# Kernel tuning notes

Measured on AMD Instinct MI355X. Metric: run time of the kernel, lower is better.

## Reference

```python
import jax, jax.numpy as jnp
import numpy as np

D_MODEL = 512
D_STATE = 16
EXPAND = 2
DT_RANK = 8
D_INNER = EXPAND * D_MODEL  # 1024
LN_EPS = 1e-5


def setup_inputs() -> dict:
    key = jax.random.key(0)
    ks = jax.random.split(key, 10)
    B, H, W = 8, 48, 48
    inp = {
        "x": jax.random.normal(ks[0], (B, H, W, D_MODEL), jnp.float32),
        # Linear weights stored [in, out] (torch weight transposed)
        "W_in": jax.random.normal(ks[1], (D_MODEL, 2 * D_INNER), jnp.float32) * 0.02,
        # depthwise conv kernel, HWIO with feature_group_count = D_INNER
        "conv_k": jax.random.normal(ks[2], (3, 3, 1, D_INNER), jnp.float32) * 0.1,
        "W_xproj": jax.random.normal(ks[3], (D_INNER, DT_RANK + 2 * D_STATE), jnp.float32) * 0.02,
        "W_dt": jax.random.uniform(ks[4], (DT_RANK, D_INNER), jnp.float32, -0.1, 0.1),
        "b_dt": jnp.full((D_INNER,), 0.1, jnp.float32),
        "A_log": jax.random.normal(ks[5], (D_STATE,), jnp.float32) * 0.02,
        "Dskip": jnp.ones((D_INNER,), jnp.float32),
        "W_dtN": jax.random.normal(ks[6], (D_INNER, D_STATE), jnp.float32) * 0.02,
        "b_dtN": jnp.zeros((D_STATE,), jnp.float32),
        "ln_g": jnp.ones((D_INNER,), jnp.float32),
        "ln_b": jnp.zeros((D_INNER,), jnp.float32),
        "W_out": jax.random.normal(ks[7], (D_INNER, D_MODEL), jnp.float32) * 0.02,
        "b_out": jnp.zeros((D_MODEL,), jnp.float32),
    }
    return inp


def _ss2d(x, W_in, conv_k, W_xproj, W_dt, b_dt, A_log, Dskip, W_dtN, b_dtN,
          ln_g, ln_b, W_out, b_out):
    B, H, W_, _ = x.shape
    L = H * W_
    # in_proj and split into x / gate z
    xz = x @ W_in                                   # [B,H,W,2*D_INNER]
    xh, z = jnp.split(xz, 2, axis=-1)
    # depthwise 3x3 conv (NHWC)
    xc = jax.lax.conv_general_dilated(
        xh, conv_k, window_strides=(1, 1), padding='SAME',
        dimension_numbers=('NHWC', 'HWIO', 'NHWC'),
        feature_group_count=D_INNER)                 # [B,H,W,D_INNER]
    # x_proj -> (dt_rank, B, C)
    xp = xc @ W_xproj
    dt_r = xp[..., :DT_RANK]
    Bp = xp[..., DT_RANK:DT_RANK + D_STATE]
    Cp = xp[..., DT_RANK + D_STATE:]
    dt = dt_r @ W_dt + b_dt                          # [B,H,W,D_INNER]
    # flatten spatial dims into sequence
    x_seq = xc.reshape(B, L, D_INNER)
    dt_seq = jax.nn.softplus(dt.reshape(B, L, D_INNER))
    B_seq = Bp.reshape(B, L, D_STATE)
    C_seq = Cp.reshape(B, L, D_STATE)
    A = -jnp.exp(A_log)                              # [N]; A_log expanded over D is constant per-row
    dtN = dt_seq @ W_dtN + b_dtN                     # dt_to_N_proj(softplus(dt)) -> [B,L,N]

    def step(h, t):
        x_t, dt_t, dtN_t, B_t, C_t = t               # [B,D],[B,D],[B,N],[B,N],[B,N]
        dA = jnp.exp(dt_t[:, :, None] * A)           # [B,D,N]
        dB = dtN_t * B_t                             # [B,N]
        h = dA * h + dB[:, None, :] * x_t[:, :, None]  # [B,D,N]
        y = jnp.einsum('bdn,bn->bd', h, C_t) + Dskip * x_t
        return h, y

    h0 = jnp.zeros((B, D_INNER, D_STATE), x.dtype)
    xs = (x_seq.transpose(1, 0, 2), dt_seq.transpose(1, 0, 2),
          dtN.transpose(1, 0, 2), B_seq.transpose(1, 0, 2),
          C_seq.transpose(1, 0, 2))
    _, ys = jax.lax.scan(step, h0, xs)               # ys: [L,B,D]
    y = ys.transpose(1, 0, 2).reshape(B, H, W_, D_INNER)
    # LayerNorm over channel dim
    mu = y.mean(-1, keepdims=True)
    var = ((y - mu) ** 2).mean(-1, keepdims=True)
    y = (y - mu) / jnp.sqrt(var + LN_EPS) * ln_g + ln_b
    # gate and out projection (dropout = identity in eval)
    y = y * jax.nn.silu(z)
    return y @ W_out + b_out


def reference(x, W_in, conv_k, W_xproj, W_dt, b_dt, A_log, Dskip, W_dtN,
              b_dtN, ln_g, ln_b, W_out, b_out):
    return _ss2d(x, W_in, conv_k, W_xproj, W_dt, b_dt, A_log, Dskip, W_dtN,
                 b_dtN, ln_g, ln_b, W_out, b_out)
```

## Files before the change

kernel.cpp:

```cpp
#include <hip/hip_runtime.h>
#include <hip/hip_bf16.h>

#define NBATCH 8
#define HEIGHT 48
#define WIDTH  48
#define DMODEL 512
#define DSTATE 16
#define DTRANK 8
#define DINNER 1024
#define LSEQ   (HEIGHT*WIDTH)
#define NROWS  (NBATCH*LSEQ)
#define NXP    40
#define NCH    32
#define TCH    72

typedef unsigned short u16;
typedef unsigned int   u32;
typedef __attribute__((ext_vector_type(8))) short short8;
typedef __attribute__((ext_vector_type(4))) float f32x4;

__device__ __forceinline__ float bf2f(u16 u) {
    u32 x = ((u32)u) << 16;
    return __uint_as_float(x);
}
__device__ __forceinline__ u16 f2bf(float f) {
    u32 x = __float_as_uint(f);
    u32 r = (x + 0x7FFFu + ((x >> 16) & 1u)) >> 16;
    return (u16)r;
}

#if __has_builtin(__builtin_amdgcn_exp2f)
__device__ __forceinline__ float EXP2(float x) { return __builtin_amdgcn_exp2f(x); }
#else
__device__ __forceinline__ float EXP2(float x) { return __expf(x * 0.69314718f); }
#endif

#define GLD16(g, l) __builtin_amdgcn_global_load_lds( \
    (const __attribute__((address_space(1))) void*)(g), \
    (__attribute__((address_space(3))) void*)(l), 16, 0, 0)

__global__ __launch_bounds__(256) void k_prep_x(const float* __restrict__ x,
                                                u16* __restrict__ xbf) {
    int i = blockIdx.x * 256 + threadIdx.x;
    float4 v = *reinterpret_cast<const float4*>(x + (size_t)i * 4);
    ushort4 o;
    o.x = f2bf(v.x); o.y = f2bf(v.y); o.z = f2bf(v.z); o.w = f2bf(v.w);
    *reinterpret_cast<ushort4*>(xbf + (size_t)i * 4) = o;
}

__global__ __launch_bounds__(256) void k_prep_w(const float* __restrict__ W_in,
                                                const float* __restrict__ W_out,
                                                const float* __restrict__ W_xproj,
                                                const float* __restrict__ W_dtN,
                                                u16* __restrict__ WinT,
                                                u16* __restrict__ WoutT,
                                                u16* __restrict__ WxpB,
                                                u16* __restrict__ WdtNB) {
    int idx = blockIdx.x * 256 + threadIdx.x;
    if (idx < 2048 * 512) {
        int n = idx >> 9, k = idx & 511;
        WinT[idx] = f2bf(W_in[(size_t)k * 2048 + n]);
    } else if (idx < 2048 * 512 + 512 * 1024) {
        int j = idx - 2048 * 512;
        int n = j >> 10, k = j & 1023;
        WoutT[j] = f2bf(W_out[(size_t)k * 512 + n]);
    } else if (idx < 2048 * 512 + 512 * 1024 + 48 * 1024) {
        int j = idx - (2048 * 512 + 512 * 1024);
        int n = j >> 10, k = j & 1023;
        WxpB[j] = (n < NXP) ? f2bf(W_xproj[(size_t)k * NXP + n]) : (u16)0;
    } else {
        int j = idx - (2048 * 512 + 512 * 1024 + 48 * 1024);
        int n = j >> 10, k = j & 1023;
        WdtNB[j] = f2bf(W_dtN[(size_t)k * DSTATE + n]);
    }
}

template<int K, int LDA, int LDB, int LDC, bool F32OUT>
__global__ __launch_bounds__(256) void k_gemm_mfma(const u16* __restrict__ A,
                                                   const u16* __restrict__ B,
                                                   const float* __restrict__ bias,
                                                   void* __restrict__ Cv) {
    __shared__ u16 As[128 * 32];
    __shared__ u16 Bs[128 * 32];
    const int tid = threadIdx.x;
    const int l   = tid & 63;
    const int w   = tid >> 6;
    const int wm  = w >> 1, wn = w & 1;
    const int m0  = blockIdx.y * 128, n0 = blockIdx.x * 128;
    const int srow = w * 32 + (l >> 2);
    const int sc   = l & 3;
    const int kh = l >> 4;
    const int lr = l & 15;

    f32x4 acc[4][4];
#pragma unroll
    for (int i = 0; i < 4; ++i)
#pragma unroll
        for (int j = 0; j < 4; ++j)
            acc[i][j] = (f32x4){0.f, 0.f, 0.f, 0.f};

    for (int k0 = 0; k0 < K; k0 += 32) {
#pragma unroll
        for (int i = 0; i < 2; ++i) {
            int r  = srow + i * 16;
            int cg = sc ^ ((r >> 1) & 3);
            const u16* ga = A + (size_t)(m0 + r) * LDA + k0 + cg * 8;
            const u16* gb = B + (size_t)(n0 + r) * LDB + k0 + cg * 8;
            GLD16(ga, As + (w * 2 + i) * 512);
            GLD16(gb, Bs + (w * 2 + i) * 512);
        }
        __syncthreads();
        short8 af[4], bfr[4];
#pragma unroll
        for (int f = 0; f < 4; ++f) {
            int ar = wm * 64 + f * 16 + lr;
            af[f]  = *reinterpret_cast<const short8*>(As + ar * 32 + ((kh ^ ((ar >> 1) & 3)) * 8));
            int br = wn * 64 + f * 16 + lr;
            bfr[f] = *reinterpret_cast<const short8*>(Bs + br * 32 + ((kh ^ ((br >> 1) & 3)) * 8));
        }
#pragma unroll
        for (int fm = 0; fm < 4; ++fm)
#pragma unroll
            for (int fn = 0; fn < 4; ++fn)
                acc[fm][fn] = __builtin_amdgcn_mfma_f32_16x16x32_bf16(
                    af[fm], bfr[fn], acc[fm][fn], 0, 0, 0);
        __syncthreads();
    }

#pragma unroll
    for (int fm = 0; fm < 4; ++fm) {
#pragma unroll
        for (int r = 0; r < 4; ++r) {
            int row = m0 + wm * 64 + fm * 16 + (l >> 4) * 4 + r;
#pragma unroll
            for (int fn = 0; fn < 4; ++fn) {
                int col = n0 + wn * 64 + fn * 16 + lr;
                if (F32OUT) {
                    ((float*)Cv)[(size_t)row * LDC + col] = acc[fm][fn][r] + bias[col];
                } else {
                    ((u16*)Cv)[(size_t)row * LDC + col] = f2bf(acc[fm][fn][r]);
                }
            }
        }
    }
}

__global__ __launch_bounds__(256) void k_conv(const u16* __restrict__ xz,
                                              const float* __restrict__ ck,
                                              u16* __restrict__ xc) {
    int row = blockIdx.x;
    int w = row % WIDTH;
    int hb = row / WIDTH;
    int h = hb % HEIGHT;
    int b = hb / HEIGHT;
    int c0 = threadIdx.x * 4;
    float a0 = 0.f, a1 = 0.f, a2 = 0.f, a3 = 0.f;
#pragma unroll
    for (int kh = 0; kh < 3; ++kh) {
        int hh = h + kh - 1;
        if (hh < 0 || hh >= HEIGHT) continue;
#pragma unroll
        for (int kw = 0; kw < 3; ++kw) {
            int ww = w + kw - 1;
            if (ww < 0 || ww >= WIDTH) continue;
            int r = (b * HEIGHT + hh) * WIDTH + ww;
            ushort4 v = *reinterpret_cast<const ushort4*>(xz + (size_t)r * 2048 + c0);
            float4 kv = *reinterpret_cast<const float4*>(ck + (kh * 3 + kw) * DINNER + c0);
            a0 = fmaf(bf2f(v.x), kv.x, a0);
            a1 = fmaf(bf2f(v.y), kv.y, a1);
            a2 = fmaf(bf2f(v.z), kv.z, a2);
            a3 = fmaf(bf2f(v.w), kv.w, a3);
        }
    }
    ushort4 ov;
    ov.x = f2bf(a0); ov.y = f2bf(a1); ov.z = f2bf(a2); ov.w = f2bf(a3);
    *reinterpret_cast<ushort4*>(xc + (size_t)row * DINNER + c0) = ov;
}

__global__ __launch_bounds__(256) void k_xproj(const u16* __restrict__ xc,
                                               const u16* __restrict__ WxpB,
                                               float* __restrict__ xp_out) {
    __shared__ u16 As[64 * 32];
    __shared__ u16 Bs[48 * 32];
    const int tid = threadIdx.x;
    const int l = tid & 63;
    const int w = tid >> 6;
    const int m0 = blockIdx.x * 64;
    const int kh = l >> 4, lr = l & 15;
    const int srow = w * 16 + (l >> 2);
    const int sc = l & 3;

    f32x4 acc[3];
    acc[0] = acc[1] = acc[2] = (f32x4){0.f, 0.f, 0.f, 0.f};

    for (int k0 = 0; k0 < 1024; k0 += 32) {
        {
            int cg = sc ^ ((srow >> 1) & 3);
            GLD16(xc + (size_t)(m0 + srow) * DINNER + k0 + cg * 8, As + w * 512);
            if (w < 3)
                GLD16(WxpB + (size_t)srow * 1024 + k0 + cg * 8, Bs + w * 512);
        }
        __syncthreads();
        int ar = w * 16 + lr;
        short8 af = *reinterpret_cast<const short8*>(As + ar * 32 + ((kh ^ ((ar >> 1) & 3)) * 8));
#pragma unroll
        for (int fn = 0; fn < 3; ++fn) {
            int br = fn * 16 + lr;
            short8 bf = *reinterpret_cast<const short8*>(Bs + br * 32 + ((kh ^ ((br >> 1) & 3)) * 8));
            acc[fn] = __builtin_amdgcn_mfma_f32_16x16x32_bf16(af, bf, acc[fn], 0, 0, 0);
        }
        __syncthreads();
    }
#pragma unroll
    for (int fn = 0; fn < 3; ++fn)
#pragma unroll
        for (int r = 0; r < 4; ++r) {
            int row = m0 + w * 16 + (l >> 4) * 4 + r;
            int col = fn * 16 + lr;
            if (col < NXP) xp_out[(size_t)row * NXP + col] = acc[fn][r];
        }
}

__global__ __launch_bounds__(256) void k_dt(const float* __restrict__ xp,
                                            const float* __restrict__ W_dt,
                                            const float* __restrict__ b_dt,
                                            u16* __restrict__ dt_out) {
    int gid = blockIdx.x * 256 + threadIdx.x;
    int row = gid >> 7;
    int dj  = (gid & 127) * 8;
    const float* xr = xp + (size_t)row * NXP;
    float4 xa = *reinterpret_cast<const float4*>(xr);
    float4 xb = *reinterpret_cast<const float4*>(xr + 4);
    float xv[8] = {xa.x, xa.y, xa.z, xa.w, xb.x, xb.y, xb.z, xb.w};
    float a[8];
    {
        float4 b0 = *reinterpret_cast<const float4*>(b_dt + dj);
        float4 b1 = *reinterpret_cast<const float4*>(b_dt + dj + 4);
        a[0]=b0.x; a[1]=b0.y; a[2]=b0.z; a[3]=b0.w;
        a[4]=b1.x; a[5]=b1.y; a[6]=b1.z; a[7]=b1.w;
    }
#pragma unroll
    for (int j = 0; j < 8; ++j) {
        float4 w0 = *reinterpret_cast<const float4*>(W_dt + j * DINNER + dj);
        float4 w1 = *reinterpret_cast<const float4*>(W_dt + j * DINNER + dj + 4);
        a[0] = fmaf(xv[j], w0.x, a[0]); a[1] = fmaf(xv[j], w0.y, a[1]);
        a[2] = fmaf(xv[j], w0.z, a[2]); a[3] = fmaf(xv[j], w0.w, a[3]);
        a[4] = fmaf(xv[j], w1.x, a[4]); a[5] = fmaf(xv[j], w1.y, a[5]);
        a[6] = fmaf(xv[j], w1.z, a[6]); a[7] = fmaf(xv[j], w1.w, a[7]);
    }
    short8 o;
#pragma unroll
    for (int j = 0; j < 8; ++j) {
        float dt = fmaxf(a[j], 0.f) + log1pf(__expf(-fabsf(a[j])));
        o[j] = (short)f2bf(dt);
    }
    *reinterpret_cast<short8*>(dt_out + (size_t)row * DINNER + dj) = o;
}

__global__ __launch_bounds__(256) void k_dtn(const u16* __restrict__ dtb,
                                             const u16* __restrict__ WdtNB,
                                             const float* __restrict__ b_dtN,
                                             const float* __restrict__ xp,
                                             float* __restrict__ dnBC) {
    __shared__ u16 As[64 * 32];
    __shared__ u16 Bs[16 * 32];
    const int tid = threadIdx.x;
    const int l = tid & 63;
    const int w = tid >> 6;
    const int m0 = blockIdx.x * 64;
    const int kh = l >> 4, lr = l & 15;
    const int srow = w * 16 + (l >> 2);
    const int sc = l & 3;

    f32x4 acc = (f32x4){0.f, 0.f, 0.f, 0.f};

    for (int k0 = 0; k0 < 1024; k0 += 32) {
        {
            int cg = sc ^ ((srow >> 1) & 3);
            GLD16(dtb + (size_t)(m0 + srow) * DINNER + k0 + cg * 8, As + w * 512);
            if (w == 0)
                GLD16(WdtNB + (size_t)srow * 1024 + k0 + cg * 8, Bs);
        }
        __syncthreads();
        int ar = w * 16 + lr;
        short8 af = *reinterpret_cast<const short8*>(As + ar * 32 + ((kh ^ ((ar >> 1) & 3)) * 8));
        short8 bf = *reinterpret_cast<const short8*>(Bs + lr * 32 + ((kh ^ ((lr >> 1) & 3)) * 8));
        acc = __builtin_amdgcn_mfma_f32_16x16x32_bf16(af, bf, acc, 0, 0, 0);
        __syncthreads();
    }
    float bn = b_dtN[lr];
#pragma unroll
    for (int r = 0; r < 4; ++r) {
        int row = m0 + w * 16 + (l >> 4) * 4 + r;
        float dn = acc[r] + bn;
        float Bv = xp[(size_t)row * NXP + DTRANK + lr];
        float Cv = xp[(size_t)row * NXP + DTRANK + DSTATE + lr];
        dnBC[(size_t)row * 32 + lr]      = dn * Bv;
        dnBC[(size_t)row * 32 + 16 + lr] = Cv;
    }
}

__global__ __launch_bounds__(256) void k_scan_p1(const u16* __restrict__ xc,
                                                 const u16* __restrict__ dtb,
                                                 const float* __restrict__ dnBC,
                                                 const float* __restrict__ A_log,
                                                 float* __restrict__ Pbuf,
                                                 float* __restrict__ Qbuf) {
    const int tid = threadIdx.x;
    const int blk = blockIdx.x;
    const int quarter = blk & 3;
    const int bc = blk >> 2;
    const int c = bc & (NCH - 1);
    const int b = bc >> 5;
    const int d = quarter * 256 + tid;

    float An2[16];
#pragma unroll
    for (int n = 0; n < 16; ++n)
        An2[n] = -__expf(A_log[n]) * 1.44269504f;

    float h[16];
#pragma unroll
    for (int n = 0; n < 16; ++n) h[n] = 0.f;
    float sdt = 0.f;

    const size_t row0 = (size_t)b * LSEQ + (size_t)c * TCH;
#pragma unroll 4
    for (int t = 0; t < TCH; ++t) {
        size_t row = row0 + t;
        float dt = bf2f(dtb[row * DINNER + d]);
        float xt = bf2f(xc[row * DINNER + d]);
        const float4* dv = reinterpret_cast<const float4*>(dnBC + row * 32);
        float4 u0 = dv[0], u1 = dv[1], u2 = dv[2], u3 = dv[3];
        sdt += dt;
        float u[16] = {u0.x,u0.y,u0.z,u0.w, u1.x,u1.y,u1.z,u1.w,
                       u2.x,u2.y,u2.z,u2.w, u3.x,u3.y,u3.z,u3.w};
#pragma unroll
        for (int n = 0; n < 16; ++n) {
            float dA = EXP2(dt * An2[n]);
            h[n] = fmaf(dA, h[n], u[n] * xt);
        }
    }
    size_t base = ((size_t)bc << 14) + d;
#pragma unroll
    for (int n = 0; n < 16; ++n) {
        Pbuf[base + (size_t)n * DINNER] = EXP2(sdt * An2[n]);
        Qbuf[base + (size_t)n * DINNER] = h[n];
    }
}

__global__ __launch_bounds__(256) void k_scan_p2(const float* __restrict__ Pbuf,
                                                 float* __restrict__ Qbuf) {
    int tid = blockIdx.x * 256 + threadIdx.x;
    int b = tid >> 14, rem = tid & 16383;
    float h = 0.f;
    for (int c = 0; c < NCH; ++c) {
        size_t idx = ((size_t)(b * NCH + c) << 14) + rem;
        float P = Pbuf[idx];
        float q = Qbuf[idx];
        Qbuf[idx] = h;
        h = fmaf(P, h, q);
    }
}

__global__ __launch_bounds__(256) void k_scan_p3(const u16* __restrict__ xc,
                                                 const u16* __restrict__ dtb,
                                                 const float* __restrict__ dnBC,
                                                 const float* __restrict__ A_log,
                                                 const float* __restrict__ Dskip,
                                                 const float* __restrict__ Qbuf,
                                                 u16* __restrict__ ybuf) {
    const int tid = threadIdx.x;
    const int blk = blockIdx.x;
    const int quarter = blk & 3;
    const int bc = blk >> 2;
    const int c = bc & (NCH - 1);
    const int b = bc >> 5;
    const int d = quarter * 256 + tid;

    float An2[16];
#pragma unroll
    for (int n = 0; n < 16; ++n)
        An2[n] = -__expf(A_log[n]) * 1.44269504f;

    float h[16];
    size_t base = ((size_t)bc << 14) + d;
#pragma unroll
    for (int n = 0; n < 16; ++n) h[n] = Qbuf[base + (size_t)n * DINNER];
    float Dsk = Dskip[d];

    const size_t row0 = (size_t)b * LSEQ + (size_t)c * TCH;
#pragma unroll 2
    for (int t = 0; t < TCH; ++t) {
        size_t row = row0 + t;
        float dt = bf2f(dtb[row * DINNER + d]);
        float xt = bf2f(xc[row * DINNER + d]);
        const float4* sv = reinterpret_cast<const float4*>(dnBC + row * 32);
        float4 u0 = sv[0], u1 = sv[1], u2 = sv[2], u3 = sv[3];
        float4 c0 = sv[4], c1 = sv[5], c2 = sv[6], c3 = sv[7];
        float u[16]  = {u0.x,u0.y,u0.z,u0.w, u1.x,u1.y,u1.z,u1.w,
                        u2.x,u2.y,u2.z,u2.w, u3.x,u3.y,u3.z,u3.w};
        float cv[16] = {c0.x,c0.y,c0.z,c0.w, c1.x,c1.y,c1.z,c1.w,
                        c2.x,c2.y,c2.z,c2.w, c3.x,c3.y,c3.z,c3.w};
        float ys[4] = {Dsk * xt, 0.f, 0.f, 0.f};
#pragma unroll
        for (int n = 0; n < 16; ++n) {
            float dA = EXP2(dt * An2[n]);
            h[n] = fmaf(dA, h[n], u[n] * xt);
            ys[n & 3] = fmaf(h[n], cv[n], ys[n & 3]);
        }
        ybuf[row * 2048 + d] = f2bf((ys[0] + ys[1]) + (ys[2] + ys[3]));
    }
}

__global__ __launch_bounds__(256) void k_ln_gate(u16* __restrict__ xz,
                                                 const float* __restrict__ ln_g,
                                                 const float* __restrict__ ln_b) {
    __shared__ float red[8];
    int row = blockIdx.x, tid = threadIdx.x;
    u16* yrow = xz + (size_t)row * 2048;
    int c0 = tid * 4;
    ushort4 v = *reinterpret_cast<const ushort4*>(yrow + c0);
    float y0 = bf2f(v.x), y1 = bf2f(v.y), y2 = bf2f(v.z), y3 = bf2f(v.w);
    float s = y0 + y1 + y2 + y3;
    float q = y0 * y0 + y1 * y1 + y2 * y2 + y3 * y3;
#pragma unroll
    for (int m = 32; m; m >>= 1) {
        s += __shfl_xor(s, m, 64);
        q += __shfl_xor(q, m, 64);
    }
    int lane = tid & 63, wv = tid >> 6;
    if (lane == 0) { red[wv] = s; red[4 + wv] = q; }
    __syncthreads();
    s = red[0] + red[1] + red[2] + red[3];
    q = red[4] + red[5] + red[6] + red[7];
    float mu = s * (1.f / DINNER);
    float var = q * (1.f / DINNER) - mu * mu;
    float rstd = rsqrtf(var + 1e-5f);
    ushort4 zv = *reinterpret_cast<const ushort4*>(yrow + DINNER + c0);
    float4 lg = *reinterpret_cast<const float4*>(ln_g + c0);
    float4 lb = *reinterpret_cast<const float4*>(ln_b + c0);
    float z0 = bf2f(zv.x), z1 = bf2f(zv.y), z2 = bf2f(zv.z), z3 = bf2f(zv.w);
    float g0 = ((y0 - mu) * rstd * lg.x + lb.x) * (z0 / (1.f + __expf(-z0)));
    float g1 = ((y1 - mu) * rstd * lg.y + lb.y) * (z1 / (1.f + __expf(-z1)));
    float g2 = ((y2 - mu) * rstd * lg.z + lb.z) * (z2 / (1.f + __expf(-z2)));
    float g3 = ((y3 - mu) * rstd * lg.w + lb.w) * (z3 / (1.f + __expf(-z3)));
    ushort4 ov;
    ov.x = f2bf(g0); ov.y = f2bf(g1); ov.z = f2bf(g2); ov.w = f2bf(g3);
    *reinterpret_cast<ushort4*>(yrow + c0) = ov;
}

extern "C" void kernel_launch(void* const* d_in, const int* in_sizes, int n_in,
                              void* d_out, int out_size, void* d_ws, size_t ws_size,
                              hipStream_t stream) {
    const float* x       = (const float*)d_in[0];
    const float* W_in    = (const float*)d_in[1];
    const float* conv_k  = (const float*)d_in[2];
    const float* W_xproj = (const float*)d_in[3];
    const float* W_dt    = (const float*)d_in[4];
    const float* b_dt    = (const float*)d_in[5];
    const float* A_log   = (const float*)d_in[6];
    const float* Dskip   = (const float*)d_in[7];
    const float* W_dtN   = (const float*)d_in[8];
    const float* b_dtN   = (const float*)d_in[9];
    const float* ln_g    = (const float*)d_in[10];
    const float* ln_b    = (const float*)d_in[11];
    const float* W_out   = (const float*)d_in[12];
    const float* b_out   = (const float*)d_in[13];
    float* out = (float*)d_out;

    char* ws = (char*)d_ws;
    size_t off = 0;
    u16*   xz    = (u16*)(ws + off); off += (size_t)NROWS * 2048 * 2;
    u16*   xc    = (u16*)(ws + off); off += (size_t)NROWS * 1024 * 2;
    u16*   dtb   = (u16*)(ws + off); off += (size_t)NROWS * 1024 * 2;
    float* xpb   = (float*)(ws + off); off += (size_t)NROWS * NXP * 4;
    float* dnBC  = (float*)(ws + off); off += (size_t)NROWS * 32 * 4;
    char*  scr   = ws + off; off += 2 * (size_t)NBATCH * NCH * DINNER * DSTATE * 4;
    u16*   xbf   = (u16*)scr;
    float* Pbuf  = (float*)scr;
    float* Qbuf  = (float*)(scr + (size_t)NBATCH * NCH * DINNER * DSTATE * 4);
    u16*   WinT  = (u16*)(ws + off); off += (size_t)2048 * 512 * 2;
    u16*   WoutT = (u16*)(ws + off); off += (size_t)512 * 1024 * 2;
    u16*   WxpB  = (u16*)(ws + off); off += (size_t)48 * 1024 * 2;
    u16*   WdtNB = (u16*)(ws + off); off += (size_t)16 * 1024 * 2;

    k_prep_x<<<(NROWS * DMODEL / 4) / 256, 256, 0, stream>>>(x, xbf);
    k_prep_w<<<(2048 * 512 + 512 * 1024 + 48 * 1024 + 16 * 1024) / 256, 256, 0, stream>>>(
        W_in, W_out, W_xproj, W_dtN, WinT, WoutT, WxpB, WdtNB);
    k_gemm_mfma<512, 512, 512, 2048, false>
        <<<dim3(2048 / 128, NROWS / 128), 256, 0, stream>>>(xbf, WinT, nullptr, xz);
    k_conv<<<NROWS, 256, 0, stream>>>(xz, conv_k, xc);
    k_xproj<<<NROWS / 64, 256, 0, stream>>>(xc, WxpB, xpb);
    k_dt<<<(NROWS * DINNER / 8) / 256, 256, 0, stream>>>(xpb, W_dt, b_dt, dtb);
    k_dtn<<<NROWS / 64, 256, 0, stream>>>(dtb, WdtNB, b_dtN, xpb, dnBC);
    k_scan_p1<<<NBATCH * NCH * 4, 256, 0, stream>>>(xc, dtb, dnBC, A_log,
                                                    Pbuf, Qbuf);
    k_scan_p2<<<(NBATCH * DINNER * DSTATE) / 256, 256, 0, stream>>>(Pbuf, Qbuf);
    k_scan_p3<<<NBATCH * NCH * 4, 256, 0, stream>>>(xc, dtb, dnBC, A_log,
                                                    Dskip, Qbuf, xz);
    k_ln_gate<<<NROWS, 256, 0, stream>>>(xz, ln_g, ln_b);
    k_gemm_mfma<1024, 2048, 1024, 512, true>
        <<<dim3(DMODEL / 128, NROWS / 128), 256, 0, stream>>>(xz, WoutT, b_out, out);
}
```

Measured before the change: 363.1 us.

## Split scan state dimension across two half-waves to double scan parallelism

The chunked scan kernels (p1 and p3) now split the 16 state components between two 32-lane halves of each wavefront, so each thread carries 8 states instead of 16, and the grid doubles to 8 blocks per (batch, chunk). In p3 the partial outputs are combined with a cross-half shuffle and only one half writes y. This halves per-thread serial work and register pressure and doubles the number of blocks, at the cost of duplicated dt/x loads and extra shuffles.

```diff
diff --git a/kernel.cpp b/kernel.cpp
--- a/kernel.cpp
+++ b/kernel.cpp
@@ -308,20 +308,25 @@
                                                  float* __restrict__ Qbuf) {
     const int tid = threadIdx.x;
     const int blk = blockIdx.x;
-    const int quarter = blk & 3;
-    const int bc = blk >> 2;
+    const int oct = blk & 7;
+    const int bc  = blk >> 3;
     const int c = bc & (NCH - 1);
     const int b = bc >> 5;
-    const int d = quarter * 256 + tid;
-
-    float An2[16];
-#pragma unroll
-    for (int n = 0; n < 16; ++n)
-        An2[n] = -__expf(A_log[n]) * 1.44269504f;
-
-    float h[16];
-#pragma unroll
-    for (int n = 0; n < 16; ++n) h[n] = 0.f;
+    const int w = tid >> 6;
+    const int lane = tid & 63;
+    const int dL = lane & 31;
+    const int nh = lane >> 5;
+    const int d = oct * 128 + w * 32 + dL;
+    const int nb = nh * 8;
+
+    float An2[8];
+#pragma unroll
+    for (int j = 0; j < 8; ++j)
+        An2[j] = -__expf(A_log[nb + j]) * 1.44269504f;
+
+    float h[8];
+#pragma unroll
+    for (int j = 0; j < 8; ++j) h[j] = 0.f;
     float sdt = 0.f;
 
     const size_t row0 = (size_t)b * LSEQ + (size_t)c * TCH;
@@ -330,22 +335,21 @@
         size_t row = row0 + t;
         float dt = bf2f(dtb[row * DINNER + d]);
         float xt = bf2f(xc[row * DINNER + d]);
-        const float4* dv = reinterpret_cast<const float4*>(dnBC + row * 32);
-        float4 u0 = dv[0], u1 = dv[1], u2 = dv[2], u3 = dv[3];
+        const float4* dv = reinterpret_cast<const float4*>(dnBC + row * 32 + nb);
+        float4 u0 = dv[0], u1 = dv[1];
         sdt += dt;
-        float u[16] = {u0.x,u0.y,u0.z,u0.w, u1.x,u1.y,u1.z,u1.w,
-                       u2.x,u2.y,u2.z,u2.w, u3.x,u3.y,u3.z,u3.w};
-#pragma unroll
-        for (int n = 0; n < 16; ++n) {
-            float dA = EXP2(dt * An2[n]);
-            h[n] = fmaf(dA, h[n], u[n] * xt);
-        }
-    }
-    size_t base = ((size_t)bc << 14) + d;
-#pragma unroll
-    for (int n = 0; n < 16; ++n) {
-        Pbuf[base + (size_t)n * DINNER] = EXP2(sdt * An2[n]);
-        Qbuf[base + (size_t)n * DINNER] = h[n];
+        float u[8] = {u0.x, u0.y, u0.z, u0.w, u1.x, u1.y, u1.z, u1.w};
+#pragma unroll
+        for (int j = 0; j < 8; ++j) {
+            float dA = EXP2(dt * An2[j]);
+            h[j] = fmaf(dA, h[j], u[j] * xt);
+        }
+    }
+    size_t base = ((size_t)bc << 14) + (size_t)nb * DINNER + d;
+#pragma unroll
+    for (int j = 0; j < 8; ++j) {
+        Pbuf[base + (size_t)j * DINNER] = EXP2(sdt * An2[j]);
+        Qbuf[base + (size_t)j * DINNER] = h[j];
     }
 }
 
@@ -372,21 +376,26 @@
                                                  u16* __restrict__ ybuf) {
     const int tid = threadIdx.x;
     const int blk = blockIdx.x;
-    const int quarter = blk & 3;
-    const int bc = blk >> 2;
+    const int oct = blk & 7;
+    const int bc  = blk >> 3;
     const int c = bc & (NCH - 1);
     const int b = bc >> 5;
-    const int d = quarter * 256 + tid;
-
-    float An2[16];
-#pragma unroll
-    for (int n = 0; n < 16; ++n)
-        An2[n] = -__expf(A_log[n]) * 1.44269504f;
-
-    float h[16];
-    size_t base = ((size_t)bc << 14) + d;
-#pragma unroll
-    for (int n = 0; n < 16; ++n) h[n] = Qbuf[base + (size_t)n * DINNER];
+    const int w = tid >> 6;
+    const int lane = tid & 63;
+    const int dL = lane & 31;
+    const int nh = lane >> 5;
+    const int d = oct * 128 + w * 32 + dL;
+    const int nb = nh * 8;
+
+    float An2[8];
+#pragma unroll
+    for (int j = 0; j < 8; ++j)
+        An2[j] = -__expf(A_log[nb + j]) * 1.44269504f;
+
+    float h[8];
+    size_t base = ((size_t)bc << 14) + (size_t)nb * DINNER + d;
+#pragma unroll
+    for (int j = 0; j < 8; ++j) h[j] = Qbuf[base + (size_t)j * DINNER];
     float Dsk = Dskip[d];
 
     const size_t row0 = (size_t)b * LSEQ + (size_t)c * TCH;
@@ -395,21 +404,22 @@
         size_t row = row0 + t;
         float dt = bf2f(dtb[row * DINNER + d]);
         float xt = bf2f(xc[row * DINNER + d]);
-        const float4* sv = reinterpret_cast<const float4*>(dnBC + row * 32);
-        float4 u0 = sv[0], u1 = sv[1], u2 = sv[2], u3 = sv[3];
-        float4 c0 = sv[4], c1 = sv[5], c2 = sv[6], c3 = sv[7];
-        float u[16]  = {u0.x,u0.y,u0.z,u0.w, u1.x,u1.y,u1.z,u1.w,
-                        u2.x,u2.y,u2.z,u2.w, u3.x,u3.y,u3.z,u3.w};
-        float cv[16] = {c0.x,c0.y,c0.z,c0.w, c1.x,c1.y,c1.z,c1.w,
-                        c2.x,c2.y,c2.z,c2.w, c3.x,c3.y,c3.z,c3.w};
-        float ys[4] = {Dsk * xt, 0.f, 0.f, 0.f};
-#pragma unroll
-        for (int n = 0; n < 16; ++n) {
-            float dA = EXP2(dt * An2[n]);
-            h[n] = fmaf(dA, h[n], u[n] * xt);
-            ys[n & 3] = fmaf(h[n], cv[n], ys[n & 3]);
-        }
-        ybuf[row * 2048 + d] = f2bf((ys[0] + ys[1]) + (ys[2] + ys[3]));
+        const float4* uv = reinterpret_cast<const float4*>(dnBC + row * 32 + nb);
+        const float4* cvp = reinterpret_cast<const float4*>(dnBC + row * 32 + 16 + nb);
+        float4 u0 = uv[0], u1 = uv[1];
+        float4 c0 = cvp[0], c1 = cvp[1];
+        float u[8]  = {u0.x, u0.y, u0.z, u0.w, u1.x, u1.y, u1.z, u1.w};
+        float cv[8] = {c0.x, c0.y, c0.z, c0.w, c1.x, c1.y, c1.z, c1.w};
+        float ys[4] = {0.f, 0.f, 0.f, 0.f};
+#pragma unroll
+        for (int j = 0; j < 8; ++j) {
+            float dA = EXP2(dt * An2[j]);
+            h[j] = fmaf(dA, h[j], u[j] * xt);
+            ys[j & 3] = fmaf(h[j], cv[j], ys[j & 3]);
+        }
+        float p = (ys[0] + ys[1]) + (ys[2] + ys[3]);
+        p += __shfl_xor(p, 32, 64);
+        if (nh == 0) ybuf[row * 2048 + d] = f2bf(p + Dsk * xt);
     }
 }
 
@@ -494,10 +504,10 @@
     k_xproj<<<NROWS / 64, 256, 0, stream>>>(xc, WxpB, xpb);
     k_dt<<<(NROWS * DINNER / 8) / 256, 256, 0, stream>>>(xpb, W_dt, b_dt, dtb);
     k_dtn<<<NROWS / 64, 256, 0, stream>>>(dtb, WdtNB, b_dtN, xpb, dnBC);
-    k_scan_p1<<<NBATCH * NCH * 4, 256, 0, stream>>>(xc, dtb, dnBC, A_log,
+    k_scan_p1<<<NBATCH * NCH * 8, 256, 0, stream>>>(xc, dtb, dnBC, A_log,
                                                     Pbuf, Qbuf);
     k_scan_p2<<<(NBATCH * DINNER * DSTATE) / 256, 256, 0, stream>>>(Pbuf, Qbuf);
-    k_scan_p3<<<NBATCH * NCH * 4, 256, 0, stream>>>(xc, dtb, dnBC, A_log,
+    k_scan_p3<<<NBATCH * NCH * 8, 256, 0, stream>>>(xc, dtb, dnBC, A_log,
                                                     Dskip, Qbuf, xz);
     k_ln_gate<<<NROWS, 256, 0, stream>>>(xz, ln_g, ln_b);
     k_gemm_mfma<1024, 2048, 1024, 512, true>
```

New measurement: 419.2 us. 1.15x slower.
